# Kernel tuning notes

Hardware: AMD Instinct MI355X
Metric: run time of the kernel (lower is better)

## Reference

```python
import jax, jax.numpy as jnp
import numpy as np

B, S, H, P2 = 64, 512, 768, 46  # batch, seq, hidden, num_p*2


def setup_inputs() -> dict:
    key = jax.random.key(0)
    k1, k2, k3, k4 = jax.random.split(key, 4)
    hidden_states = jax.random.normal(k1, (B, S, H), dtype=jnp.float32)
    # subject start/end indices must lie within the valid (masked-in) prefix
    lengths = jax.random.randint(k2, (B,), S // 4, S + 1)  # cue lengths per sample
    input_mask = (jnp.arange(S)[None, :] < lengths[:, None]).astype(jnp.int32)
    ids = jax.random.randint(k3, (B, 2), 0, S // 4)
    batch_subject_ids = jnp.sort(ids, axis=1).astype(jnp.int32)
    W = jax.random.normal(k4, (P2, H), dtype=jnp.float32) * (1.0 / np.sqrt(H))
    b = jnp.zeros((P2,), dtype=jnp.float32)
    return {"hidden_states": hidden_states, "batch_subject_ids": batch_subject_ids,
            "input_mask": input_mask, "W": W, "b": b}


def reference(hidden_states, batch_subject_ids, input_mask, W, b):
    # per-sample subject embedding: h[b, start] + h[b, end]  -> [B, H]
    batch_idx = jnp.arange(hidden_states.shape[0])
    s = (hidden_states[batch_idx, batch_subject_ids[:, 0]]
         + hidden_states[batch_idx, batch_subject_ids[:, 1]])
    # broadcast-add s to the first cue_len positions of each sample
    cue_len = jnp.sum(input_mask, axis=1)  # [B]
    pos_mask = (jnp.arange(hidden_states.shape[1])[None, :] < cue_len[:, None])  # [B, S]
    h = hidden_states + s[:, None, :] * pos_mask[:, :, None].astype(hidden_states.dtype)
    # linear + sigmoid^4 (dropout is identity in eval mode)
    logits = jnp.einsum('bsh,ph->bsp', h, W) + b
    return jax.nn.sigmoid(logits) ** 4
```

## Files before the change

### kernel.cpp

```cpp
#include <hip/hip_runtime.h>

#define SEQ 512
#define HID 768
#define P2  46
#define NTP 48
#define MT  64
#define KC  64
#define BLK 256
#define NCHUNK (HID / KC)

typedef short bf16x8 __attribute__((ext_vector_type(8)));
typedef float f32x4  __attribute__((ext_vector_type(4)));

__device__ __forceinline__ unsigned short f2bf(float f) {
  union { float f; unsigned int u; } v; v.f = f;
  return (unsigned short)((v.u + 0x7FFFu + ((v.u >> 16) & 1u)) >> 16);
}

__global__ __launch_bounds__(64) void qk_kernel(const float* __restrict__ h,
                                                const int* __restrict__ ids,
                                                const float* __restrict__ W,
                                                float* __restrict__ q) {
  int b = blockIdx.x, p = blockIdx.y;
  int lane = threadIdx.x;
  int i0 = ids[b * 2 + 0], i1 = ids[b * 2 + 1];
  const float* r0 = h + ((size_t)b * SEQ + i0) * HID;
  const float* r1 = h + ((size_t)b * SEQ + i1) * HID;
  const float* w  = W + (size_t)p * HID;
  float acc = 0.f;
  #pragma unroll
  for (int j = 0; j < HID / 64; ++j) {
    int k = lane + j * 64;
    acc += (r0[k] + r1[k]) * w[k];
  }
  #pragma unroll
  for (int off = 32; off > 0; off >>= 1)
    acc += __shfl_down(acc, off, 64);
  if (lane == 0) q[b * P2 + p] = acc;
}

__global__ __launch_bounds__(BLK) void gemm_kernel(const float* __restrict__ h,
                                                   const int* __restrict__ mask,
                                                   const float* __restrict__ W,
                                                   const float* __restrict__ bias,
                                                   const float* __restrict__ q,
                                                   float* __restrict__ out) {
  __shared__ __align__(16) unsigned short hA[2][MT][72];
  __shared__ __align__(16) unsigned short wB[2][NTP][72];

  const int tid  = threadIdx.x;
  const int row0 = blockIdx.x * MT;
  const int b    = row0 >> 9;
  const int lane = tid & 63, wv = tid >> 6;
  const int mr = lane & 15, qd = lane >> 4;

  float4 hreg[4];
  float4 wreg[3];

  auto loadH = [&](int c) {
    int k0 = c * KC;
    #pragma unroll
    for (int i = 0; i < 4; ++i) {
      int idx = tid + i * BLK;
      int r = idx >> 4, c4 = idx & 15;
      hreg[i] = *(const float4*)(h + ((size_t)(row0 + r)) * HID + k0 + c4 * 4);
    }
  };
  auto loadW = [&](int c) {
    int k0 = c * KC;
    #pragma unroll
    for (int i = 0; i < 3; ++i) {
      int idx = tid + i * BLK;
      int r = idx >> 4, c4 = idx & 15;
      if (r < P2)
        wreg[i] = *(const float4*)(W + (size_t)r * HID + k0 + c4 * 4);
      else
        wreg[i] = make_float4(0.f, 0.f, 0.f, 0.f);
    }
  };
  auto storeH = [&](int buf) {
    #pragma unroll
    for (int i = 0; i < 4; ++i) {
      int idx = tid + i * BLK;
      int r = idx >> 4, c4 = idx & 15;
      ushort4 v;
      v.x = f2bf(hreg[i].x); v.y = f2bf(hreg[i].y);
      v.z = f2bf(hreg[i].z); v.w = f2bf(hreg[i].w);
      *(ushort4*)&hA[buf][r][c4 * 4] = v;
    }
  };
  auto storeW = [&](int buf) {
    #pragma unroll
    for (int i = 0; i < 3; ++i) {
      int idx = tid + i * BLK;
      int r = idx >> 4, c4 = idx & 15;
      ushort4 v;
      v.x = f2bf(wreg[i].x); v.y = f2bf(wreg[i].y);
      v.z = f2bf(wreg[i].z); v.w = f2bf(wreg[i].w);
      *(ushort4*)&wB[buf][r][c4 * 4] = v;
    }
  };

  f32x4 acc[3];
  #pragma unroll
  for (int nt = 0; nt < 3; ++nt) acc[nt] = f32x4{0.f, 0.f, 0.f, 0.f};

  auto compute = [&](int buf) {
    #pragma unroll
    for (int ks = 0; ks < 2; ++ks) {
      bf16x8 a = *(const bf16x8*)&hA[buf][(wv << 4) + mr][ks * 32 + (qd << 3)];
      #pragma unroll
      for (int nt = 0; nt < 3; ++nt) {
        bf16x8 bb = *(const bf16x8*)&wB[buf][(nt << 4) + mr][ks * 32 + (qd << 3)];
        acc[nt] = __builtin_amdgcn_mfma_f32_16x16x32_bf16(a, bb, acc[nt], 0, 0, 0);
      }
    }
  };

  loadH(0); loadW(0);
  storeH(0); storeW(0);
  __syncthreads();

  for (int c = 0; c < NCHUNK; ++c) {
    int cur = c & 1;
    if (c + 1 < NCHUNK) { loadH(c + 1); loadW(c + 1); }
    compute(cur);
    if (c + 1 < NCHUNK) { storeH(cur ^ 1); storeW(cur ^ 1); }
    __syncthreads();
  }

  int mrow[4];
  #pragma unroll
  for (int i = 0; i < 4; ++i)
    mrow[i] = mask[row0 + (wv << 4) + (qd << 2) + i];

  #pragma unroll
  for (int nt = 0; nt < 3; ++nt) {
    int p = (nt << 4) + mr;
    if (p < P2) {
      float bv = bias[p];
      float qv = q[b * P2 + p];
      #pragma unroll
      for (int i = 0; i < 4; ++i) {
        int row = row0 + (wv << 4) + (qd << 2) + i;
        float x = acc[nt][i] + bv + (mrow[i] ? qv : 0.f);
        float sg = 1.f / (1.f + __expf(-x));
        sg *= sg; sg *= sg;
        out[(size_t)row * P2 + p] = sg;
      }
    }
  }
}

extern "C" void kernel_launch(void* const* d_in, const int* in_sizes, int n_in,
                              void* d_out, int out_size, void* d_ws, size_t ws_size,
                              hipStream_t stream) {
  const float* h    = (const float*)d_in[0];
  const int*   ids  = (const int*)d_in[1];
  const int*   mask = (const int*)d_in[2];
  const float* W    = (const float*)d_in[3];
  const float* bias = (const float*)d_in[4];
  float* out = (float*)d_out;
  float* q   = (float*)d_ws;

  qk_kernel<<<dim3(64, P2), 64, 0, stream>>>(h, ids, W, q);
  gemm_kernel<<<dim3((64 * SEQ) / MT), BLK, 0, stream>>>(h, mask, W, bias, q, out);
}
```

Before: 161.8 us.

## Load activations straight to MFMA registers and stage W in LDS by halves

The GEMM kernel no longer double-buffers activation tiles through LDS. Each lane now loads its A fragment directly from global memory into registers (24 float4 per half) and converts it to bf16 in place. W is converted and staged into LDS in two halves of 384 columns, with only three barriers in total. This removes the LDS round trip and most synchronisation for the activation stream. In exchange it raises register pressure, gives up overlap between loading and compute, and does strided per-lane global reads instead of coalesced tile loads.

```diff
diff --git a/kernel.cpp b/kernel.cpp
--- a/kernel.cpp
+++ b/kernel.cpp
@@ -3,11 +3,9 @@
 #define SEQ 512
 #define HID 768
 #define P2  46
-#define NTP 48
-#define MT  64
-#define KC  64
 #define BLK 256
-#define NCHUNK (HID / KC)
+#define KH  384
+#define WST 392
 
 typedef short bf16x8 __attribute__((ext_vector_type(8)));
 typedef float f32x4  __attribute__((ext_vector_type(4)));
@@ -45,89 +43,65 @@
                                                    const float* __restrict__ bias,
                                                    const float* __restrict__ q,
                                                    float* __restrict__ out) {
-  __shared__ __align__(16) unsigned short hA[2][MT][72];
-  __shared__ __align__(16) unsigned short wB[2][NTP][72];
+  __shared__ __align__(16) unsigned short wlds[48 * WST];
 
   const int tid  = threadIdx.x;
-  const int row0 = blockIdx.x * MT;
+  const int lane = tid & 63, wv = tid >> 6;
+  const int mr   = lane & 15, qd = lane >> 4;
+  const int row0 = blockIdx.x * 64;
   const int b    = row0 >> 9;
-  const int lane = tid & 63, wv = tid >> 6;
-  const int mr = lane & 15, qd = lane >> 4;
-
-  float4 hreg[4];
-  float4 wreg[3];
-
-  auto loadH = [&](int c) {
-    int k0 = c * KC;
-    #pragma unroll
-    for (int i = 0; i < 4; ++i) {
-      int idx = tid + i * BLK;
-      int r = idx >> 4, c4 = idx & 15;
-      hreg[i] = *(const float4*)(h + ((size_t)(row0 + r)) * HID + k0 + c4 * 4);
-    }
-  };
-  auto loadW = [&](int c) {
-    int k0 = c * KC;
-    #pragma unroll
-    for (int i = 0; i < 3; ++i) {
-      int idx = tid + i * BLK;
-      int r = idx >> 4, c4 = idx & 15;
-      if (r < P2)
-        wreg[i] = *(const float4*)(W + (size_t)r * HID + k0 + c4 * 4);
-      else
-        wreg[i] = make_float4(0.f, 0.f, 0.f, 0.f);
-    }
-  };
-  auto storeH = [&](int buf) {
-    #pragma unroll
-    for (int i = 0; i < 4; ++i) {
-      int idx = tid + i * BLK;
-      int r = idx >> 4, c4 = idx & 15;
-      ushort4 v;
-      v.x = f2bf(hreg[i].x); v.y = f2bf(hreg[i].y);
-      v.z = f2bf(hreg[i].z); v.w = f2bf(hreg[i].w);
-      *(ushort4*)&hA[buf][r][c4 * 4] = v;
-    }
-  };
-  auto storeW = [&](int buf) {
-    #pragma unroll
-    for (int i = 0; i < 3; ++i) {
-      int idx = tid + i * BLK;
-      int r = idx >> 4, c4 = idx & 15;
-      ushort4 v;
-      v.x = f2bf(wreg[i].x); v.y = f2bf(wreg[i].y);
-      v.z = f2bf(wreg[i].z); v.w = f2bf(wreg[i].w);
-      *(ushort4*)&wB[buf][r][c4 * 4] = v;
-    }
-  };
+  const int rowa = row0 + (wv << 4) + mr;
+  const float* hrow = h + (size_t)rowa * HID + (qd << 3);
 
   f32x4 acc[3];
   #pragma unroll
   for (int nt = 0; nt < 3; ++nt) acc[nt] = f32x4{0.f, 0.f, 0.f, 0.f};
 
-  auto compute = [&](int buf) {
+  auto stageW = [&](int half) {
+    for (int i = tid; i < (2 * WST) / 2; i += BLK)
+      ((unsigned int*)(wlds + 46 * WST))[i] = 0u;
+    for (int i = tid; i < (P2 * KH) / 4; i += BLK) {
+      int f = i * 4;
+      int r = f / KH;
+      int c = f - r * KH;
+      float4 w4 = *(const float4*)(W + (size_t)r * HID + half * KH + c);
+      ushort4 v;
+      v.x = f2bf(w4.x); v.y = f2bf(w4.y); v.z = f2bf(w4.z); v.w = f2bf(w4.w);
+      *(ushort4*)&wlds[r * WST + c] = v;
+    }
+  };
+
+  auto phase = [&](int half) {
+    const float* hb = hrow + half * KH;
+    float4 abuf[24];
     #pragma unroll
-    for (int ks = 0; ks < 2; ++ks) {
-      bf16x8 a = *(const bf16x8*)&hA[buf][(wv << 4) + mr][ks * 32 + (qd << 3)];
+    for (int i = 0; i < 24; ++i)
+      abuf[i] = *(const float4*)(hb + (i >> 1) * 32 + (i & 1) * 4);
+    #pragma unroll
+    for (int it = 0; it < 12; ++it) {
+      bf16x8 a;
+      {
+        float4 x0 = abuf[2 * it], x1 = abuf[2 * it + 1];
+        a[0] = (short)f2bf(x0.x); a[1] = (short)f2bf(x0.y);
+        a[2] = (short)f2bf(x0.z); a[3] = (short)f2bf(x0.w);
+        a[4] = (short)f2bf(x1.x); a[5] = (short)f2bf(x1.y);
+        a[6] = (short)f2bf(x1.z); a[7] = (short)f2bf(x1.w);
+      }
       #pragma unroll
       for (int nt = 0; nt < 3; ++nt) {
-        bf16x8 bb = *(const bf16x8*)&wB[buf][(nt << 4) + mr][ks * 32 + (qd << 3)];
+        bf16x8 bb = *(const bf16x8*)&wlds[((nt << 4) + mr) * WST + it * 32 + (qd << 3)];
         acc[nt] = __builtin_amdgcn_mfma_f32_16x16x32_bf16(a, bb, acc[nt], 0, 0, 0);
       }
     }
   };
 
-  loadH(0); loadW(0);
-  storeH(0); storeW(0);
+  stageW(0);
   __syncthreads();
-
-  for (int c = 0; c < NCHUNK; ++c) {
-    int cur = c & 1;
-    if (c + 1 < NCHUNK) { loadH(c + 1); loadW(c + 1); }
-    compute(cur);
-    if (c + 1 < NCHUNK) { storeH(cur ^ 1); storeW(cur ^ 1); }
-    __syncthreads();
-  }
+  phase(0);
+  __syncthreads();
+  stageW(1);
+  __syncthreads();
+  phase(1);
 
   int mrow[4];
   #pragma unroll
@@ -164,5 +138,5 @@
   float* q   = (float*)d_ws;
 
   qk_kernel<<<dim3(64, P2), 64, 0, stream>>>(h, ids, W, q);
-  gemm_kernel<<<dim3((64 * SEQ) / MT), BLK, 0, stream>>>(h, mask, W, bias, q, out);
+  gemm_kernel<<<dim3((64 * SEQ) / 64), BLK, 0, stream>>>(h, mask, W, bias, q, out);
 }
```

Result: slower. 168.0 us (+3.9%).
